# Kernel optimization log

Measured on AMD Instinct MI355X. Metric: run time of the kernel, lower is better.

The kernel has to match this reference:

```python
import jax, jax.numpy as jnp
import numpy as np

B, N, F, D, H = 4, 2048, 128, 128, 4

def setup_inputs() -> dict:
    key = jax.random.key(0)
    k1, k2, k3, k4 = jax.random.split(key, 4)
    X = jax.random.normal(k1, (B, N, F), dtype=jnp.float32)
    A = jax.random.uniform(k2, (B, N, N), dtype=jnp.float32)
    kernel = jax.random.normal(k3, (F, D), dtype=jnp.float32) * 0.05
    bias = jnp.ones((D,), dtype=jnp.float32)
    attn = jax.random.normal(k4, (H, D, D), dtype=jnp.float32) * 0.05
    return {"X": X, "A": A, "kernel": kernel, "bias": bias, "attn": attn}

def reference(X, A, kernel, bias, attn):
    # Linear projection: [B,N,F] @ [F,D] + bias -> [B,N,D]
    Xp = jnp.einsum('bnf,fd->bnd', X, kernel) + bias
    # Per-head bilinear scores Xp @ attn_h @ Xp^T, batched over heads: [B,H,N,N]
    scores = jnp.einsum('bnd,hde,bme->bhnm', Xp, attn, Xp)
    # Adjacency mask + tanh (fused elementwise)
    Am = jnp.tanh(A[:, None, :, :] * scores)
    # Weighted aggregate per head: [B,H,N,N] @ [B,N,D] -> [B,H,N,D]
    heads = jnp.einsum('bhnm,bmd->bhnd', Am, Xp)
    # Mean over heads, relu
    Xh = jax.nn.relu(jnp.mean(heads, axis=1))
    # Skip connection (shapes match since F == D): relu(Xh + X)
    out = jax.nn.relu(Xh + X)
    return out
```

## Files before the change

### kernel.cpp

```cpp
#include <hip/hip_runtime.h>

#define NB 4
#define NN 2048
#define ND 128
#define NH 4

typedef short short8 __attribute__((ext_vector_type(8)));
typedef short short4v __attribute__((ext_vector_type(4)));
typedef float floatx4 __attribute__((ext_vector_type(4)));

__device__ __forceinline__ short f2bf(float f){
  unsigned u = __float_as_uint(f);
  u += 0x7FFFu + ((u >> 16) & 1u);
  return (short)(u >> 16);
}
__device__ __forceinline__ float bf2f(short s){
  unsigned u = ((unsigned)(unsigned short)s) << 16;
  return __uint_as_float(u);
}

__global__ __launch_bounds__(256) void k1_xp(const float* __restrict__ X,
                                             const float* __restrict__ W,
                                             const float* __restrict__ bias,
                                             short* __restrict__ Xp,
                                             short* __restrict__ XpT){
  int bid = blockIdx.x;
  int b = bid >> 5, i0 = (bid & 31) << 6;
  int t = threadIdx.x, w = t >> 6, lane = t & 63, lq = lane >> 4, lc = lane & 15;
  __shared__ __align__(16) short ldsB[16384];
  for (int k = 0; k < 64; ++k){
    int idx = k * 256 + t; int f = idx >> 7, d = idx & 127;
    ldsB[((f >> 3) * 128 + d) * 8 + (f & 7)] = f2bf(W[idx]);
  }
  short8 af[4][4];
  #pragma unroll
  for (int ib = 0; ib < 4; ++ib)
    #pragma unroll
    for (int k = 0; k < 4; ++k){
      const float* xp = &X[(b * NN + i0 + ib * 16 + lc) * ND + k * 32 + lq * 8];
      float4 x0 = *(const float4*)xp;
      float4 x1 = *(const float4*)(xp + 4);
      short8 s;
      s[0]=f2bf(x0.x); s[1]=f2bf(x0.y); s[2]=f2bf(x0.z); s[3]=f2bf(x0.w);
      s[4]=f2bf(x1.x); s[5]=f2bf(x1.y); s[6]=f2bf(x1.z); s[7]=f2bf(x1.w);
      af[ib][k] = s;
    }
  __syncthreads();
  floatx4 acc[4][2];
  #pragma unroll
  for (int ib = 0; ib < 4; ++ib)
    #pragma unroll
    for (int eb = 0; eb < 2; ++eb) acc[ib][eb] = (floatx4){0.f, 0.f, 0.f, 0.f};
  #pragma unroll
  for (int eb = 0; eb < 2; ++eb)
    #pragma unroll
    for (int k = 0; k < 4; ++k){
      short8 bf = *(short8*)&ldsB[(k * 4 + lq) * 1024 + (w * 32 + eb * 16 + lc) * 8];
      #pragma unroll
      for (int ib = 0; ib < 4; ++ib)
        acc[ib][eb] = __builtin_amdgcn_mfma_f32_16x16x32_bf16(af[ib][k], bf, acc[ib][eb], 0, 0, 0);
    }
  __syncthreads();
  short* tr = ldsB;
  #pragma unroll
  for (int ib = 0; ib < 4; ++ib)
    #pragma unroll
    for (int eb = 0; eb < 2; ++eb){
      int d = w * 32 + eb * 16 + lc;
      float bv = bias[d];
      #pragma unroll
      for (int r = 0; r < 4; ++r){
        int n = i0 + ib * 16 + lq * 4 + r;
        short s = f2bf(acc[ib][eb][r] + bv);
        Xp[(b * NN + n) * ND + d] = s;
        tr[d * 72 + (n - i0)] = s;
      }
    }
  __syncthreads();
  #pragma unroll
  for (int c = 0; c < 4; ++c){
    int g = c * 256 + t; int d = g >> 3, n8 = g & 7;
    short8 v;
    #pragma unroll
    for (int j = 0; j < 8; ++j) v[j] = tr[d * 72 + n8 * 8 + j];
    *(short8*)&XpT[(b * ND + d) * NN + i0 + n8 * 8] = v;
  }
}

__global__ __launch_bounds__(256) void k2_y(const short* __restrict__ Xp,
                                            const float* __restrict__ attn,
                                            short* __restrict__ Y){
  int bid = blockIdx.x;
  int it = bid & 31, h = (bid >> 5) & 3, b = bid >> 7;
  int i0 = it << 6;
  int t = threadIdx.x, w = t >> 6, lane = t & 63, lq = lane >> 4, lc = lane & 15;
  __shared__ __align__(16) short ldsB[16384];
  const float* Asrc = attn + h * 16384;
  for (int k = 0; k < 64; ++k){
    int idx = k * 256 + t; int dd = idx >> 7, e = idx & 127;
    ldsB[((dd >> 3) * 128 + e) * 8 + (dd & 7)] = f2bf(Asrc[idx]);
  }
  short8 af[4][4];
  #pragma unroll
  for (int ib = 0; ib < 4; ++ib)
    #pragma unroll
    for (int k = 0; k < 4; ++k)
      af[ib][k] = *(const short8*)&Xp[(b * NN + i0 + ib * 16 + lc) * ND + k * 32 + lq * 8];
  __syncthreads();
  floatx4 acc[4][2];
  #pragma unroll
  for (int ib = 0; ib < 4; ++ib)
    #pragma unroll
    for (int eb = 0; eb < 2; ++eb) acc[ib][eb] = (floatx4){0.f, 0.f, 0.f, 0.f};
  #pragma unroll
  for (int eb = 0; eb < 2; ++eb)
    #pragma unroll
    for (int k = 0; k < 4; ++k){
      short8 bf = *(short8*)&ldsB[(k * 4 + lq) * 1024 + (w * 32 + eb * 16 + lc) * 8];
      #pragma unroll
      for (int ib = 0; ib < 4; ++ib)
        acc[ib][eb] = __builtin_amdgcn_mfma_f32_16x16x32_bf16(af[ib][k], bf, acc[ib][eb], 0, 0, 0);
    }
  #pragma unroll
  for (int ib = 0; ib < 4; ++ib)
    #pragma unroll
    for (int eb = 0; eb < 2; ++eb){
      int e = w * 32 + eb * 16 + lc;
      #pragma unroll
      for (int r = 0; r < 4; ++r){
        int n = i0 + ib * 16 + lq * 4 + r;
        Y[((b * NH + h) * NN + n) * ND + e] = f2bf(acc[ib][eb][r]);
      }
    }
}

__global__ __launch_bounds__(256, 4) void k3_fused(const short* __restrict__ Xp,
                                                   const short* __restrict__ XpT,
                                                   const short* __restrict__ Y,
                                                   const float* __restrict__ A,
                                                   float* __restrict__ part){
  int bid = blockIdx.x;
  int it = bid & 127, b = (bid >> 7) & 3, ms = bid >> 9;
  int i0 = it << 4;
  int t = threadIdx.x, w = t >> 6, lane = t & 63, lq = lane >> 4, lc = lane & 15;

  __shared__ __align__(16) short ldsY[8192];
  __shared__ __align__(16) short ldsXpT[8320];
  __shared__ __align__(16) short ldsPh[1024];
  __shared__ __align__(16) short ldsPl[1024];

  #pragma unroll
  for (int c = 0; c < 4; ++c){
    int slot = c * 256 + t;
    int h = slot >> 8, i = (slot >> 4) & 15, d8 = slot & 15;
    short8 v = *(const short8*)&Y[((b * NH + h) * NN + i0 + i) * ND + d8 * 8];
    *(short8*)&ldsY[h * 2048 + i * 128 + ((d8 ^ (i & 7)) << 3)] = v;
  }

  floatx4 acc[2];
  acc[0] = (floatx4){0.f,0.f,0.f,0.f};
  acc[1] = (floatx4){0.f,0.f,0.f,0.f};

  const int mbase = ms << 9;
  const int poff = (w * 2 + (lq >> 1)) * 128 + lc * 8 + (lq & 1) * 4;

  __syncthreads();

  for (int itn = 0; itn < 8; ++itn){
    int m0 = mbase + itn * 64;
    if (itn) __syncthreads();
    const short* src = XpT + b * (ND * NN) + m0;
    #pragma unroll
    for (int c = 0; c < 4; ++c){
      int q = c * 256 + t; int d = q >> 3, mb = q & 7;
      *(short8*)&ldsXpT[mb * 1040 + d * 8] = *(const short8*)&src[d * NN + mb * 8];
    }
    short8 xpf[4];
    const short* xr = Xp + (b * NN + m0 + w * 16 + lc) * ND;
    #pragma unroll
    for (int k = 0; k < 4; ++k) xpf[k] = *(const short8*)&xr[k * 32 + lq * 8];
    floatx4 av = *(const floatx4*)&A[(size_t)(b * NN + i0 + lc) * NN + m0 + w * 16 + lq * 4];

    float psum[4] = {0.f, 0.f, 0.f, 0.f};
    #pragma unroll
    for (int h = 0; h < 4; ++h){
      floatx4 S = (floatx4){0.f,0.f,0.f,0.f};
      #pragma unroll
      for (int k = 0; k < 4; ++k){
        short8 yfr = *(short8*)&ldsY[h * 2048 + lc * 128 + (((k * 4 + lq) ^ (lc & 7)) << 3)];
        S = __builtin_amdgcn_mfma_f32_16x16x32_bf16(xpf[k], yfr, S, 0, 0, 0);
      }
      #pragma unroll
      for (int r = 0; r < 4; ++r){
        float x = av[r] * S[r];
        float e = __builtin_amdgcn_exp2f(x * 2.885390081777926f);
        psum[r] += 1.f - 2.f * __builtin_amdgcn_rcpf(e + 1.f);
      }
    }
    short4v hi4, lo4;
    #pragma unroll
    for (int r = 0; r < 4; ++r){
      float pb = 0.25f * psum[r];
      short h16 = f2bf(pb);
      hi4[r] = h16;
      lo4[r] = f2bf(pb - bf2f(h16));
    }
    *(short4v*)&ldsPh[poff] = hi4;
    *(short4v*)&ldsPl[poff] = lo4;
    __syncthreads();

    #pragma unroll
    for (int kb = 0; kb < 2; ++kb){
      short8 ph = *(short8*)&ldsPh[(kb * 4 + lq) * 128 + lc * 8];
      short8 pl = *(short8*)&ldsPl[(kb * 4 + lq) * 128 + lc * 8];
      #pragma unroll
      for (int db = 0; db < 2; ++db){
        short8 bfr = *(short8*)&ldsXpT[(kb * 4 + lq) * 1040 + (w * 32 + db * 16 + lc) * 8];
        acc[db] = __builtin_amdgcn_mfma_f32_16x16x32_bf16(ph, bfr, acc[db], 0, 0, 0);
        acc[db] = __builtin_amdgcn_mfma_f32_16x16x32_bf16(pl, bfr, acc[db], 0, 0, 0);
      }
    }
  }
  float* dst = part + (size_t)ms * 1048576 + (b * NN + i0) * ND;
  #pragma unroll
  for (int db = 0; db < 2; ++db)
    #pragma unroll
    for (int r = 0; r < 4; ++r)
      dst[(lq * 4 + r) * ND + w * 32 + db * 16 + lc] = acc[db][r];
}

__global__ void k4_final(const float* __restrict__ part, const float* __restrict__ X,
                         float* __restrict__ out){
  int f = (blockIdx.x * 256 + threadIdx.x) * 4;
  float4 s0 = *(const float4*)(part + f);
  float4 s1 = *(const float4*)(part + 1048576 + f);
  float4 s2 = *(const float4*)(part + 2097152 + f);
  float4 s3 = *(const float4*)(part + 3145728 + f);
  float4 xv = *(const float4*)(X + f);
  float4 o;
  o.x = fmaxf(fmaxf(s0.x + s1.x + s2.x + s3.x, 0.f) + xv.x, 0.f);
  o.y = fmaxf(fmaxf(s0.y + s1.y + s2.y + s3.y, 0.f) + xv.y, 0.f);
  o.z = fmaxf(fmaxf(s0.z + s1.z + s2.z + s3.z, 0.f) + xv.z, 0.f);
  o.w = fmaxf(fmaxf(s0.w + s1.w + s2.w + s3.w, 0.f) + xv.w, 0.f);
  *(float4*)(out + f) = o;
}

extern "C" void kernel_launch(void* const* d_in, const int* in_sizes, int n_in,
                              void* d_out, int out_size, void* d_ws, size_t ws_size,
                              hipStream_t stream) {
  const float* X    = (const float*)d_in[0];
  const float* A    = (const float*)d_in[1];
  const float* W    = (const float*)d_in[2];
  const float* bias = (const float*)d_in[3];
  const float* attn = (const float*)d_in[4];
  float* out = (float*)d_out;

  const size_t OFF_XP    = 0;
  const size_t OFF_XPT   = (size_t)2 << 20;
  const size_t OFF_Y     = (size_t)4 << 20;
  const size_t OFF_PART  = (size_t)12 << 20;
  const size_t NEED = (size_t)28 << 20;
  if (ws_size < NEED) return;

  char* ws = (char*)d_ws;
  short* Xp    = (short*)(ws + OFF_XP);
  short* XpT   = (short*)(ws + OFF_XPT);
  short* Y     = (short*)(ws + OFF_Y);
  float* part  = (float*)(ws + OFF_PART);

  k1_xp<<<128, 256, 0, stream>>>(X, W, bias, Xp, XpT);
  k2_y<<<512, 256, 0, stream>>>(Xp, attn, Y);
  k3_fused<<<2048, 256, 0, stream>>>(Xp, XpT, Y, A, part);
  k4_final<<<1024, 256, 0, stream>>>(part, X, out);
}
```

Baseline: 168.4 us.

## Keep P tile in registers and reduce per-wave partials via LDS at end

The fused kernel no longer stages P and XpT tiles through shared memory with a barrier every m-iteration. Each wave now feeds its own 16x16 P fragment, produced in registers, straight into 16x16x16 MFMAs against XpT fragments read from global memory. Each wave accumulates the full 128-wide D output for its m-slice, and the four waves' partials are summed through LDS once at the end. This removes the per-iteration barriers and LDS traffic, at the cost of more accumulator registers, uncoalesced short4 global loads of XpT, and a final reduction.

```diff
diff --git a/kernel.cpp b/kernel.cpp
--- a/kernel.cpp
+++ b/kernel.cpp
@@ -144,10 +144,8 @@
   int i0 = it << 4;
   int t = threadIdx.x, w = t >> 6, lane = t & 63, lq = lane >> 4, lc = lane & 15;
 
-  __shared__ __align__(16) short ldsY[8192];
-  __shared__ __align__(16) short ldsXpT[8320];
-  __shared__ __align__(16) short ldsPh[1024];
-  __shared__ __align__(16) short ldsPl[1024];
+  __shared__ __align__(16) char smem[32768];
+  short* ldsY = (short*)smem;
 
   #pragma unroll
   for (int c = 0; c < 4; ++c){
@@ -156,30 +154,29 @@
     short8 v = *(const short8*)&Y[((b * NH + h) * NN + i0 + i) * ND + d8 * 8];
     *(short8*)&ldsY[h * 2048 + i * 128 + ((d8 ^ (i & 7)) << 3)] = v;
   }
-
-  floatx4 acc[2];
-  acc[0] = (floatx4){0.f,0.f,0.f,0.f};
-  acc[1] = (floatx4){0.f,0.f,0.f,0.f};
+  __syncthreads();
+
+  floatx4 acc[8];
+  #pragma unroll
+  for (int dt = 0; dt < 8; ++dt) acc[dt] = (floatx4){0.f,0.f,0.f,0.f};
 
   const int mbase = ms << 9;
-  const int poff = (w * 2 + (lq >> 1)) * 128 + lc * 8 + (lq & 1) * 4;
-
-  __syncthreads();
+  const float* arow = &A[(size_t)(b * NN + i0 + lc) * NN];
 
   for (int itn = 0; itn < 8; ++itn){
-    int m0 = mbase + itn * 64;
-    if (itn) __syncthreads();
-    const short* src = XpT + b * (ND * NN) + m0;
-    #pragma unroll
-    for (int c = 0; c < 4; ++c){
-      int q = c * 256 + t; int d = q >> 3, mb = q & 7;
-      *(short8*)&ldsXpT[mb * 1040 + d * 8] = *(const short8*)&src[d * NN + mb * 8];
-    }
+    int m0 = mbase + itn * 64 + w * 16;
+
     short8 xpf[4];
-    const short* xr = Xp + (b * NN + m0 + w * 16 + lc) * ND;
+    const short* xr = Xp + (b * NN + m0 + lc) * ND;
     #pragma unroll
     for (int k = 0; k < 4; ++k) xpf[k] = *(const short8*)&xr[k * 32 + lq * 8];
-    floatx4 av = *(const floatx4*)&A[(size_t)(b * NN + i0 + lc) * NN + m0 + w * 16 + lq * 4];
+
+    short4v xt[8];
+    #pragma unroll
+    for (int dt = 0; dt < 8; ++dt)
+      xt[dt] = *(const short4v*)&XpT[(b * ND + dt * 16 + lc) * NN + m0 + lq * 4];
+
+    floatx4 av = *(const floatx4*)&arow[m0 + lq * 4];
 
     float psum[4] = {0.f, 0.f, 0.f, 0.f};
     #pragma unroll
@@ -197,6 +194,7 @@
         psum[r] += 1.f - 2.f * __builtin_amdgcn_rcpf(e + 1.f);
       }
     }
+
     short4v hi4, lo4;
     #pragma unroll
     for (int r = 0; r < 4; ++r){
@@ -205,28 +203,28 @@
       hi4[r] = h16;
       lo4[r] = f2bf(pb - bf2f(h16));
     }
-    *(short4v*)&ldsPh[poff] = hi4;
-    *(short4v*)&ldsPl[poff] = lo4;
-    __syncthreads();
-
-    #pragma unroll
-    for (int kb = 0; kb < 2; ++kb){
-      short8 ph = *(short8*)&ldsPh[(kb * 4 + lq) * 128 + lc * 8];
-      short8 pl = *(short8*)&ldsPl[(kb * 4 + lq) * 128 + lc * 8];
-      #pragma unroll
-      for (int db = 0; db < 2; ++db){
-        short8 bfr = *(short8*)&ldsXpT[(kb * 4 + lq) * 1040 + (w * 32 + db * 16 + lc) * 8];
-        acc[db] = __builtin_amdgcn_mfma_f32_16x16x32_bf16(ph, bfr, acc[db], 0, 0, 0);
-        acc[db] = __builtin_amdgcn_mfma_f32_16x16x32_bf16(pl, bfr, acc[db], 0, 0, 0);
-      }
-    }
-  }
-  float* dst = part + (size_t)ms * 1048576 + (b * NN + i0) * ND;
-  #pragma unroll
-  for (int db = 0; db < 2; ++db)
+
+    #pragma unroll
+    for (int dt = 0; dt < 8; ++dt){
+      acc[dt] = __builtin_amdgcn_mfma_f32_16x16x16bf16_1k(hi4, xt[dt], acc[dt], 0, 0, 0);
+      acc[dt] = __builtin_amdgcn_mfma_f32_16x16x16bf16_1k(lo4, xt[dt], acc[dt], 0, 0, 0);
+    }
+  }
+
+  __syncthreads();
+  float* red = (float*)smem;
+  #pragma unroll
+  for (int dt = 0; dt < 8; ++dt)
     #pragma unroll
     for (int r = 0; r < 4; ++r)
-      dst[(lq * 4 + r) * ND + w * 32 + db * 16 + lc] = acc[db][r];
+      red[w * 2048 + (lq * 4 + r) * 128 + dt * 16 + lc] = acc[dt][r];
+  __syncthreads();
+  float* dst = part + (size_t)ms * 1048576 + (size_t)(b * NN + i0) * ND;
+  #pragma unroll
+  for (int j = 0; j < 8; ++j){
+    int idx = j * 256 + t;
+    dst[idx] = red[idx] + red[2048 + idx] + red[4096 + idx] + red[6144 + idx];
+  }
 }
 
 __global__ void k4_final(const float* __restrict__ part, const float* __restrict__ X,
```

Measured after the change: 214.8 us. +27.6%, slower.
